# Kernel tuning notes

Measured on AMD Instinct MI355X. Metric: run time of the kernel, lower is better.

Reference implementation:

```python
import jax, jax.numpy as jnp
import numpy as np

N_POINTS = 4096
N_PROJS = 2000


def setup_inputs() -> dict:
    key = jax.random.key(0)
    k1, k2, k3 = jax.random.split(key, 3)
    Xs = jax.random.normal(k1, (N_POINTS, 3), dtype=jnp.float32)
    Xt = jax.random.normal(k2, (N_POINTS, 3), dtype=jnp.float32)
    Us = jax.random.normal(k3, (N_PROJS, 3, 2), dtype=jnp.float32)
    return {"Xs": Xs, "Xt": Xt, "Us": Us}


def _project_to_circle(X, Us):
    # X: [n, d], Us: [P, d, 2] -> angles in [0, 1): [P, n]
    Xp = jnp.einsum('pdk,nd->pnk', Us, X)  # [P, n, 2]
    nrm = jnp.sqrt(jnp.sum(Xp * Xp, axis=-1, keepdims=True))
    Xp = Xp / jnp.maximum(nrm, 1e-12)  # F.normalize
    return (jnp.arctan2(-Xp[..., 1], -Xp[..., 0]) + np.pi) / (2 * np.pi)


def _emd1d_circle_p1(u_values, v_values):
    # Circular W1 via level-median (Delon et al.). u,v: [P, n], [P, m]
    P, n = u_values.shape
    m = v_values.shape[-1]
    dt = u_values.dtype
    u_w = jnp.full((P, n), 1.0 / n, dtype=dt)
    v_w = jnp.full((P, m), 1.0 / m, dtype=dt)
    us = jnp.sort(u_values, axis=-1)
    vs = jnp.sort(v_values, axis=-1)
    vals = jnp.concatenate([us, vs], axis=-1)            # [P, n+m]
    sorter = jnp.argsort(vals, axis=-1)
    vals_sorted = jnp.take_along_axis(vals, sorter, axis=-1)
    w_cat = jnp.concatenate([u_w, -v_w], axis=-1)
    cdf_diff = jnp.cumsum(jnp.take_along_axis(w_cat, sorter, axis=-1), axis=-1)
    cdf_sorter = jnp.argsort(cdf_diff, axis=-1)
    cdf_diff_sorted = jnp.take_along_axis(cdf_diff, cdf_sorter, axis=-1)
    vals_pad = jnp.concatenate([vals_sorted, jnp.ones((P, 1), dtype=dt)], axis=-1)
    delta = vals_pad[..., 1:] - vals_pad[..., :-1]
    weight_sorted = jnp.take_along_axis(delta, cdf_sorter, axis=-1)
    sum_weights = jnp.cumsum(weight_sorted, axis=-1) - 0.5
    sum_weights = jnp.where(sum_weights < 0, jnp.inf, sum_weights)
    inds = jnp.argmin(sum_weights, axis=-1)
    levMed = jnp.take_along_axis(cdf_diff_sorted, inds[:, None], axis=-1)  # [P, 1]
    return jnp.sum(delta * jnp.abs(cdf_diff - levMed), axis=-1)  # [P]


def reference(Xs, Xt, Us):
    Xps = _project_to_circle(Xs, Us)  # [P, n]
    Xpt = _project_to_circle(Xt, Us)  # [P, m]
    w1 = _emd1d_circle_p1(Xps, Xpt)
    return jnp.mean(w1)
```

## Files before the change

kernel.cpp:

```cpp
#include <hip/hip_runtime.h>
#include <math.h>

#define NPTS   4096
#define NPROJ  2000
#define NB     256
#define NMERGE 8192
#define VPT    32

__device__ __forceinline__ int sw(int i) {
    return (i & ~31) | ((i + (i >> 5)) & 31);
}

__device__ __forceinline__ void local_merge(float v[VPT], bool asc) {
    #pragma unroll
    for (int j = 16; j >= 1; j >>= 1) {
        #pragma unroll
        for (int e = 0; e < VPT; ++e) {
            if ((e & j) == 0) {
                float a = v[e], b = v[e | j];
                float mn = fminf(a, b), mx = fmaxf(a, b);
                v[e]     = asc ? mn : mx;
                v[e | j] = asc ? mx : mn;
            }
        }
    }
}

__global__ __launch_bounds__(NB, 4) void swd_kernel(
    const float* __restrict__ Xs, const float* __restrict__ Xt,
    const float* __restrict__ Us, float* __restrict__ out)
{
    __shared__ float keys[NMERGE];
    __shared__ float red[15 * 4];

    const int tid  = threadIdx.x;
    const int arr  = tid >> 7;
    const int c    = tid & 127;
    const int lane = tid & 63;
    const int wid  = tid >> 6;
    const int p    = blockIdx.x;

    const float u00 = Us[p*6+0], u01 = Us[p*6+1];
    const float u10 = Us[p*6+2], u11 = Us[p*6+3];
    const float u20 = Us[p*6+4], u21 = Us[p*6+5];

    const float pi_f   = 3.14159265358979323846f;
    const float inv2pi = 0.15915494309189535f;

    const float* __restrict__ X = arr ? Xt : Xs;

    float v[VPT];
    {
        const float4* X4 = (const float4*)(X + c * (VPT * 3));
        #pragma unroll
        for (int t = 0; t < 8; ++t) {
            float4 q0 = X4[t*3+0], q1 = X4[t*3+1], q2 = X4[t*3+2];
            #define ANG(x,y,z) ((atan2f(-((x)*u01+(y)*u11+(z)*u21), \
                                        -((x)*u00+(y)*u10+(z)*u20)) + pi_f) * inv2pi)
            v[t*4+0] = ANG(q0.x, q0.y, q0.z);
            v[t*4+1] = ANG(q0.w, q1.x, q1.y);
            v[t*4+2] = ANG(q1.z, q1.w, q2.x);
            v[t*4+3] = ANG(q2.y, q2.z, q2.w);
            #undef ANG
        }
    }

    #pragma unroll
    for (int k = 2; k <= 16; k <<= 1) {
        #pragma unroll
        for (int j = k >> 1; j >= 1; j >>= 1) {
            #pragma unroll
            for (int e = 0; e < VPT; ++e) {
                if ((e & j) == 0) {
                    bool asc = ((e & k) == 0);
                    float a = v[e], b = v[e | j];
                    float mn = fminf(a, b), mx = fmaxf(a, b);
                    v[e]     = asc ? mn : mx;
                    v[e | j] = asc ? mx : mn;
                }
            }
        }
    }

    local_merge(v, (c & 1) == 0);

    #pragma unroll
    for (int k = 64; k <= 2048; k <<= 1) {
        bool asc = ((c & (k >> 5)) == 0);
        #pragma unroll
        for (int d = k >> 6; d >= 1; d >>= 1) {
            bool keepmin = (((c & d) == 0) == asc);
            #pragma unroll
            for (int e = 0; e < VPT; ++e) {
                float o = __shfl_xor(v[e], d, 64);
                v[e] = keepmin ? fminf(v[e], o) : fmaxf(v[e], o);
            }
        }
        local_merge(v, asc);
    }

    #pragma unroll
    for (int e = 0; e < VPT; ++e) keys[sw(tid * VPT + e)] = v[e];
    __syncthreads();
    {
        const int pbase = (tid ^ 64) * VPT;
        const bool keepmin = (c & 64) == 0;
        #pragma unroll
        for (int e = 0; e < VPT; ++e) {
            float o = keys[sw(pbase + e)];
            v[e] = keepmin ? fminf(v[e], o) : fmaxf(v[e], o);
        }
    }
    __syncthreads();
    #pragma unroll
    for (int d = 32; d >= 1; d >>= 1) {
        bool keepmin = ((c & d) == 0);
        #pragma unroll
        for (int e = 0; e < VPT; ++e) {
            float o = __shfl_xor(v[e], d, 64);
            v[e] = keepmin ? fminf(v[e], o) : fmaxf(v[e], o);
        }
    }
    local_merge(v, true);

    #pragma unroll
    for (int e = 0; e < VPT; ++e) keys[sw(tid * VPT + e)] = v[e];
    __syncthreads();

    int c_init;
    unsigned int c8[8] = {0,0,0,0,0,0,0,0};
    {
        const int d0 = tid * VPT;
        int lo = d0 > NPTS ? d0 - NPTS : 0;
        int hi = d0 < NPTS ? d0 : NPTS;
        while (lo < hi) {
            int mid = (lo + hi) >> 1;
            if (keys[sw(mid)] <= keys[sw(NPTS + (d0 - 1 - mid))]) lo = mid + 1; else hi = mid;
        }
        int i = lo, j = d0 - lo;
        c_init = i - j;
        const float FMAXV = 3.402823466e+38f;
        float cu = (i < NPTS) ? keys[sw(i)] : FMAXV;
        float cv = (j < NPTS) ? keys[sw(NPTS + j)] : FMAXV;
        #pragma unroll
        for (int s = 0; s < VPT; ++s) {
            float cur;
            if (cu <= cv) { cur = cu; ++i; cu = (i < NPTS) ? keys[sw(i)] : FMAXV; }
            else          { cur = cv; ++j; cv = (j < NPTS) ? keys[sw(NPTS + j)] : FMAXV; }
            float nxt = fminf(cu, cv);
            if (nxt == FMAXV) nxt = 1.0f;
            v[s] = nxt - cur;
            int off = (i - j) - c_init;
            c8[s >> 2] |= ((unsigned int)(off & 0xff)) << ((s & 3) * 8);
        }
    }

    int lo_c = -4097, hi_c = 4096;
    #pragma unroll 1
    for (int it = 0; it < 14; ++it) {
        const int mid = (lo_c + hi_c) >> 1;
        const int thr = mid - c_init;
        float s_loc = 0.0f;
        #pragma unroll
        for (int s = 0; s < VPT; ++s) {
            int off = (int)(c8[s >> 2] << ((3 - (s & 3)) * 8)) >> 24;
            s_loc += (off <= thr) ? v[s] : 0.0f;
        }
        #pragma unroll
        for (int o = 32; o >= 1; o >>= 1) s_loc += __shfl_down(s_loc, o, 64);
        if (lane == 0) red[it * 4 + wid] = s_loc;
        __syncthreads();
        float S = red[it*4+0] + red[it*4+1] + red[it*4+2] + red[it*4+3];
        if (S >= 0.5f) hi_c = mid; else lo_c = mid;
    }
    const int cstar = hi_c;

    float part = 0.0f;
    {
        const int thr = cstar - c_init;
        #pragma unroll
        for (int s = 0; s < VPT; ++s) {
            int off = (int)(c8[s >> 2] << ((3 - (s & 3)) * 8)) >> 24;
            part += v[s] * fabsf((float)(off - thr));
        }
    }
    #pragma unroll
    for (int o = 32; o >= 1; o >>= 1) part += __shfl_down(part, o, 64);
    if (lane == 0) red[56 + wid] = part;
    __syncthreads();
    if (tid == 0) {
        float w1 = (red[56] + red[57] + red[58] + red[59]) * (1.0f / 4096.0f);
        atomicAdd(out, w1 * (1.0f / (float)NPROJ));
    }
}

extern "C" void kernel_launch(void* const* d_in, const int* in_sizes, int n_in,
                              void* d_out, int out_size, void* d_ws, size_t ws_size,
                              hipStream_t stream) {
    const float* Xs = (const float*)d_in[0];
    const float* Xt = (const float*)d_in[1];
    const float* Us = (const float*)d_in[2];
    float* out = (float*)d_out;

    hipMemsetAsync(out, 0, sizeof(float), stream);
    swd_kernel<<<NPROJ, NB, 0, stream>>>(Xs, Xt, Us, out);
}
```

Measured before the change: 238.9 us.

## Double threads per block and halve per-thread elements in bitonic sort

Raises the block size from 256 to 512 threads and cuts the elements each thread holds from 32 to 16. The bitonic network is reorganized so that the cross-wave merge stages go through shared memory, with a new swizzle function and 8-wave reductions. A sched_barrier is also added in the projection loop. The aim is lower register pressure, higher occupancy and more parallelism per projection, at the cost of extra LDS round trips and more __syncthreads calls.

```diff
diff --git a/kernel.cpp b/kernel.cpp
--- a/kernel.cpp
+++ b/kernel.cpp
@@ -3,17 +3,17 @@
 
 #define NPTS   4096
 #define NPROJ  2000
-#define NB     256
+#define NB     512
 #define NMERGE 8192
-#define VPT    32
+#define VPT    16
 
 __device__ __forceinline__ int sw(int i) {
-    return (i & ~31) | ((i + (i >> 5)) & 31);
+    return (i & ~15) | (((i & 15) + (i >> 5)) & 15);
 }
 
 __device__ __forceinline__ void local_merge(float v[VPT], bool asc) {
     #pragma unroll
-    for (int j = 16; j >= 1; j >>= 1) {
+    for (int j = VPT / 2; j >= 1; j >>= 1) {
         #pragma unroll
         for (int e = 0; e < VPT; ++e) {
             if ((e & j) == 0) {
@@ -26,16 +26,16 @@
     }
 }
 
-__global__ __launch_bounds__(NB, 4) void swd_kernel(
+__global__ __launch_bounds__(NB, 8) void swd_kernel(
     const float* __restrict__ Xs, const float* __restrict__ Xt,
     const float* __restrict__ Us, float* __restrict__ out)
 {
     __shared__ float keys[NMERGE];
-    __shared__ float red[15 * 4];
+    __shared__ float red[15 * 8];
 
     const int tid  = threadIdx.x;
-    const int arr  = tid >> 7;
-    const int c    = tid & 127;
+    const int arr  = tid >> 8;
+    const int c    = tid & 255;
     const int lane = tid & 63;
     const int wid  = tid >> 6;
     const int p    = blockIdx.x;
@@ -53,7 +53,7 @@
     {
         const float4* X4 = (const float4*)(X + c * (VPT * 3));
         #pragma unroll
-        for (int t = 0; t < 8; ++t) {
+        for (int t = 0; t < 4; ++t) {
             float4 q0 = X4[t*3+0], q1 = X4[t*3+1], q2 = X4[t*3+2];
             #define ANG(x,y,z) ((atan2f(-((x)*u01+(y)*u11+(z)*u21), \
                                         -((x)*u00+(y)*u10+(z)*u20)) + pi_f) * inv2pi)
@@ -62,11 +62,12 @@
             v[t*4+2] = ANG(q1.z, q1.w, q2.x);
             v[t*4+3] = ANG(q2.y, q2.z, q2.w);
             #undef ANG
-        }
-    }
-
-    #pragma unroll
-    for (int k = 2; k <= 16; k <<= 1) {
+            __builtin_amdgcn_sched_barrier(0);
+        }
+    }
+
+    #pragma unroll
+    for (int k = 2; k <= 8; k <<= 1) {
         #pragma unroll
         for (int j = k >> 1; j >= 1; j >>= 1) {
             #pragma unroll
@@ -85,10 +86,10 @@
     local_merge(v, (c & 1) == 0);
 
     #pragma unroll
-    for (int k = 64; k <= 2048; k <<= 1) {
-        bool asc = ((c & (k >> 5)) == 0);
-        #pragma unroll
-        for (int d = k >> 6; d >= 1; d >>= 1) {
+    for (int k = 32; k <= 1024; k <<= 1) {
+        bool asc = ((c & (k >> 4)) == 0);
+        #pragma unroll
+        for (int d = k >> 5; d >= 1; d >>= 1) {
             bool keepmin = (((c & d) == 0) == asc);
             #pragma unroll
             for (int e = 0; e < VPT; ++e) {
@@ -99,19 +100,49 @@
         local_merge(v, asc);
     }
 
-    #pragma unroll
-    for (int e = 0; e < VPT; ++e) keys[sw(tid * VPT + e)] = v[e];
-    __syncthreads();
-    {
-        const int pbase = (tid ^ 64) * VPT;
-        const bool keepmin = (c & 64) == 0;
-        #pragma unroll
-        for (int e = 0; e < VPT; ++e) {
-            float o = keys[sw(pbase + e)];
-            v[e] = keepmin ? fminf(v[e], o) : fmaxf(v[e], o);
-        }
-    }
-    __syncthreads();
+    {
+        const bool asc = ((c & 128) == 0);
+        #pragma unroll
+        for (int e = 0; e < VPT; ++e) keys[sw(tid * VPT + e)] = v[e];
+        __syncthreads();
+        {
+            const int pb = (tid ^ 64) * VPT;
+            const bool keepmin = (((c & 64) == 0) == asc);
+            #pragma unroll
+            for (int e = 0; e < VPT; ++e) {
+                float o = keys[sw(pb + e)];
+                v[e] = keepmin ? fminf(v[e], o) : fmaxf(v[e], o);
+            }
+        }
+        __syncthreads();
+        #pragma unroll
+        for (int d = 32; d >= 1; d >>= 1) {
+            bool keepmin = (((c & d) == 0) == asc);
+            #pragma unroll
+            for (int e = 0; e < VPT; ++e) {
+                float o = __shfl_xor(v[e], d, 64);
+                v[e] = keepmin ? fminf(v[e], o) : fmaxf(v[e], o);
+            }
+        }
+        local_merge(v, asc);
+    }
+
+    #pragma unroll
+    for (int D = 128; D >= 64; D >>= 1) {
+        #pragma unroll
+        for (int e = 0; e < VPT; ++e) keys[sw(tid * VPT + e)] = v[e];
+        __syncthreads();
+        {
+            const int pb = (tid ^ D) * VPT;
+            const bool keepmin = ((c & D) == 0);
+            #pragma unroll
+            for (int e = 0; e < VPT; ++e) {
+                float o = keys[sw(pb + e)];
+                v[e] = keepmin ? fminf(v[e], o) : fmaxf(v[e], o);
+            }
+        }
+        __syncthreads();
+    }
     #pragma unroll
     for (int d = 32; d >= 1; d >>= 1) {
         bool keepmin = ((c & d) == 0);
@@ -128,7 +159,7 @@
     __syncthreads();
 
     int c_init;
-    unsigned int c8[8] = {0,0,0,0,0,0,0,0};
+    unsigned int c8[4] = {0,0,0,0};
     {
         const int d0 = tid * VPT;
         int lo = d0 > NPTS ? d0 - NPTS : 0;
@@ -168,9 +199,11 @@
         }
         #pragma unroll
         for (int o = 32; o >= 1; o >>= 1) s_loc += __shfl_down(s_loc, o, 64);
-        if (lane == 0) red[it * 4 + wid] = s_loc;
-        __syncthreads();
-        float S = red[it*4+0] + red[it*4+1] + red[it*4+2] + red[it*4+3];
+        if (lane == 0) red[it * 8 + wid] = s_loc;
+        __syncthreads();
+        float S = 0.0f;
+        #pragma unroll
+        for (int w = 0; w < 8; ++w) S += red[it * 8 + w];
         if (S >= 0.5f) hi_c = mid; else lo_c = mid;
     }
     const int cstar = hi_c;
@@ -186,10 +219,11 @@
     }
     #pragma unroll
     for (int o = 32; o >= 1; o >>= 1) part += __shfl_down(part, o, 64);
-    if (lane == 0) red[56 + wid] = part;
+    if (lane == 0) red[112 + wid] = part;
     __syncthreads();
     if (tid == 0) {
-        float w1 = (red[56] + red[57] + red[58] + red[59]) * (1.0f / 4096.0f);
+        float w1 = (red[112] + red[113] + red[114] + red[115] +
+                    red[116] + red[117] + red[118] + red[119]) * (1.0f / 4096.0f);
         atomicAdd(out, w1 * (1.0f / (float)NPROJ));
     }
 }
```

Result: slower. 254.6 us (+6.5%).
